# Kernel optimization log

Hardware: AMD Instinct MI355X
Metric: run time of the kernel (lower is better)

The kernel has to match this reference:

```python
import jax, jax.numpy as jnp
import numpy as np

N_NODES = 100000
D = 128
N_EDGES = 800000


def setup_inputs() -> dict:
    key = jax.random.key(0)
    k_feat, k_src, k_dst, k_ws, k_wn = jax.random.split(key, 5)
    scale = 1.0 / np.sqrt(D)
    return {
        "features": jax.random.normal(k_feat, (N_NODES, D), jnp.float32),
        "src": jax.random.randint(k_src, (N_EDGES,), 0, N_NODES, jnp.int32),
        "dst": jax.random.randint(k_dst, (N_EDGES,), 0, N_NODES, jnp.int32),
        "gamma": jnp.ones((D,), jnp.float32),
        "beta": jnp.zeros((D,), jnp.float32),
        "W_self": jax.random.normal(k_ws, (D, D), jnp.float32) * scale,
        "W_neigh": jax.random.normal(k_wn, (D, D), jnp.float32) * scale,
        "b": jnp.zeros((D,), jnp.float32),
    }


def reference(features, src, dst, gamma, beta, W_self, W_neigh, b):
    n = features.shape[0]
    eps = 1e-5
    # BatchNorm1d (training mode: batch stats over the node dim, biased var)
    mean = jnp.mean(features, axis=0)
    var = jnp.mean(jnp.square(features - mean), axis=0)
    h = (features - mean) * jax.lax.rsqrt(var + eps) * gamma + beta  # [N, D]

    # SAGEConv 'mean': gather source feats along edges, mean-reduce per dst node
    msg = h[src]  # [E, D] irregular gather
    agg = jax.ops.segment_sum(msg, dst, num_segments=n)  # [N, D]
    deg = jax.ops.segment_sum(jnp.ones(src.shape, h.dtype), dst, num_segments=n)
    h_neigh = agg / jnp.maximum(deg, 1.0)[:, None]  # zero-degree nodes stay 0

    conv = h @ W_self + h_neigh @ W_neigh + b  # fc_self + fc_neigh + bias
    out = conv + h  # skip connection
    return jax.nn.gelu(out, approximate=False)
```

## Files before the change

kernel.cpp:

```cpp
#include <hip/hip_runtime.h>

#define DD 128
#define NPB_LOG 8
#define NPB 256
#define EPB 2048

typedef __attribute__((ext_vector_type(8))) short short8;
typedef __attribute__((ext_vector_type(4))) float f32x4;
typedef __attribute__((ext_vector_type(2))) float f32x2;

__device__ inline unsigned short f2bf(float f) {
    unsigned u = __float_as_uint(f);
    unsigned r = u + 0x7fffu + ((u >> 16) & 1u);
    return (unsigned short)(r >> 16);
}
__device__ inline float bf2f(unsigned short s) {
    return __uint_as_float(((unsigned)s) << 16);
}

__global__ __launch_bounds__(256) void phase1_k(
    const float4* __restrict__ x, float* __restrict__ stats16, int n,
    const int* __restrict__ dst, int nE, int NCHUNK, int NBUCK,
    const float* __restrict__ Wself, const float* __restrict__ Wneigh,
    unsigned short* __restrict__ Bpre, int* __restrict__ cm) {
    int b = blockIdx.x, tid = threadIdx.x;
    __shared__ float ls[8][256];
    if (b < 16) {
        int q = b * 256 + tid;
        int l = q & 63;
        int kb = ((q >> 9) << 5) + ((l >> 4) << 3);
        int nn = (((q >> 6) & 7) << 4) + (l & 15);
        bool self = (kb < 128);
        const float* Wp = self ? (Wself + (size_t)kb * 128 + nn)
                               : (Wneigh + (size_t)(kb - 128) * 128 + nn);
        unsigned tmp[4];
#pragma unroll
        for (int j = 0; j < 4; ++j) {
            float v0 = Wp[(2 * j) * 128];
            float v1 = Wp[(2 * j + 1) * 128];
            if (self) {
                if (kb + 2 * j == nn) v0 += 1.0f;
                if (kb + 2 * j + 1 == nn) v1 += 1.0f;
            }
            tmp[j] = (unsigned)f2bf(v0) | ((unsigned)f2bf(v1) << 16);
        }
        uint4 w; w.x = tmp[0]; w.y = tmp[1]; w.z = tmp[2]; w.w = tmp[3];
        *(uint4*)(Bpre + (size_t)q * 8) = w;
    } else if (b < 16 + 1024) {
        int bb = b - 16;
        int c4 = tid & 31, sub = tid >> 5;
        float sx = 0.f, sy = 0.f, sz = 0.f, sw = 0.f;
        float qx = 0.f, qy = 0.f, qz = 0.f, qw = 0.f;
        for (int r = bb * 8 + sub; r < n; r += 1024 * 8) {
            float4 v = x[(size_t)r * 32 + c4];
            sx += v.x; sy += v.y; sz += v.z; sw += v.w;
            qx += v.x * v.x; qy += v.y * v.y; qz += v.z * v.z; qw += v.w * v.w;
        }
        ls[sub][c4 * 4 + 0] = sx; ls[sub][c4 * 4 + 1] = sy;
        ls[sub][c4 * 4 + 2] = sz; ls[sub][c4 * 4 + 3] = sw;
        ls[sub][128 + c4 * 4 + 0] = qx; ls[sub][128 + c4 * 4 + 1] = qy;
        ls[sub][128 + c4 * 4 + 2] = qz; ls[sub][128 + c4 * 4 + 3] = qw;
        __syncthreads();
        float t = 0.f;
#pragma unroll
        for (int k = 0; k < 8; ++k) t += ls[k][tid];
        atomicAdd(&stats16[(bb & 15) * 256 + tid], t);
    } else {
        int chunk = b - 1040;
        int* cnt = (int*)ls;
        for (int i = tid; i < NBUCK; i += 256) cnt[i] = 0;
        __syncthreads();
        int e0 = chunk * EPB;
#pragma unroll
        for (int j = 0; j < 8; ++j) {
            int e = e0 + j * 256 + tid;
            if (e < nE) atomicAdd(&cnt[dst[e] >> NPB_LOG], 1);
        }
        __syncthreads();
        for (int bk = tid; bk < NBUCK; bk += 256)
            cm[(size_t)bk * NCHUNK + chunk] = cnt[bk];
    }
}

__global__ __launch_bounds__(256) void scanA_k(
    const int* __restrict__ v_in, int* __restrict__ bsum, int n) {
    int b = blockIdx.x, t = threadIdx.x;
    int i0 = b * 1024 + t * 4;
    int4 v = {0, 0, 0, 0};
    if (i0 + 3 < n) v = *(const int4*)(v_in + i0);
    else {
        if (i0 < n) v.x = v_in[i0];
        if (i0 + 1 < n) v.y = v_in[i0 + 1];
        if (i0 + 2 < n) v.z = v_in[i0 + 2];
    }
    __shared__ int ls[256];
    ls[t] = v.x + v.y + v.z + v.w;
    __syncthreads();
#pragma unroll
    for (int off = 128; off > 0; off >>= 1) {
        if (t < off) ls[t] += ls[t + off];
        __syncthreads();
    }
    if (t == 0) bsum[b] = ls[0];
}

__global__ __launch_bounds__(256) void scanB_k(
    const int* __restrict__ bsum, int* __restrict__ bpref,
    int* __restrict__ total_out, int nb, int n) {
    __shared__ int ls[256];
    int t = threadIdx.x;
    ls[t] = (t < nb) ? bsum[t] : 0;
    __syncthreads();
#pragma unroll
    for (int off = 1; off < 256; off <<= 1) {
        int x = (t >= off) ? ls[t - off] : 0;
        __syncthreads();
        ls[t] += x;
        __syncthreads();
    }
    if (t < nb) bpref[t] = (t == 0) ? 0 : ls[t - 1];
    if (t == nb - 1) total_out[n] = ls[t];
}

__global__ __launch_bounds__(256) void scanC_k(
    const int* __restrict__ v_in, const int* __restrict__ bpref,
    int* __restrict__ o1, int* __restrict__ o2, int n) {
    int b = blockIdx.x, t = threadIdx.x;
    int i0 = b * 1024 + t * 4;
    int4 v = {0, 0, 0, 0};
    if (i0 + 3 < n) v = *(const int4*)(v_in + i0);
    else {
        if (i0 < n) v.x = v_in[i0];
        if (i0 + 1 < n) v.y = v_in[i0 + 1];
        if (i0 + 2 < n) v.z = v_in[i0 + 2];
    }
    int s = v.x + v.y + v.z + v.w;
    __shared__ int ls[256];
    ls[t] = s;
    __syncthreads();
#pragma unroll
    for (int off = 1; off < 256; off <<= 1) {
        int x = (t >= off) ? ls[t - off] : 0;
        __syncthreads();
        ls[t] += x;
        __syncthreads();
    }
    int run = bpref[b] + ((t == 0) ? 0 : ls[t - 1]);
    int4 o;
    o.x = run; o.y = run + v.x; o.z = o.y + v.y; o.w = o.z + v.z;
    if (i0 + 3 < n) {
        *(int4*)(o1 + i0) = o;
        *(int4*)(o2 + i0) = o;
    } else {
        if (i0 < n) { o1[i0] = o.x; o2[i0] = o.x; }
        if (i0 + 1 < n) { o1[i0 + 1] = o.y; o2[i0 + 1] = o.y; }
        if (i0 + 2 < n) { o1[i0 + 2] = o.z; o2[i0 + 2] = o.z; }
    }
}

__global__ __launch_bounds__(256) void phase2_k(
    const float4* __restrict__ x, const float* __restrict__ stats16,
    const float4* __restrict__ gamma, const float4* __restrict__ beta,
    uint2* __restrict__ hbuf, unsigned* __restrict__ h8, int n, float inv_n,
    int nbNorm, const int* __restrict__ src, const int* __restrict__ dst,
    const int* __restrict__ cmscan, unsigned* __restrict__ pairs,
    int nE, int NCHUNK, int NBUCK) {
    int b = blockIdx.x, tid = threadIdx.x;
    __shared__ int shr[512];
    if (b < nbNorm) {
        float* fs = (float*)shr;
        float a = 0.f;
#pragma unroll
        for (int sh = 0; sh < 16; ++sh) a += stats16[sh * 256 + tid];
        fs[tid] = a;
        __syncthreads();
        int c4 = tid & 31, sub = tid >> 5;
        int row = b * 8 + sub;
        float4 sm = ((const float4*)fs)[c4], sq = ((const float4*)fs)[32 + c4];
        float4 g = gamma[c4], bt = beta[c4];
        float mx = sm.x * inv_n, my = sm.y * inv_n, mz = sm.z * inv_n, mw = sm.w * inv_n;
        float vx = sq.x * inv_n - mx * mx, vy = sq.y * inv_n - my * my;
        float vz = sq.z * inv_n - mz * mz, vw = sq.w * inv_n - mw * mw;
        float scx = rsqrtf(vx + 1e-5f) * g.x, scy = rsqrtf(vy + 1e-5f) * g.y;
        float scz = rsqrtf(vz + 1e-5f) * g.z, scw = rsqrtf(vw + 1e-5f) * g.w;
        float shx = bt.x - mx * scx, shy = bt.y - my * scy;
        float shz = bt.z - mz * scz, shw = bt.w - mw * scw;
        if (row < n) {
            float4 v = x[(size_t)row * 32 + c4];
            float hx = v.x * scx + shx, hy = v.y * scy + shy;
            float hz = v.z * scz + shz, hw = v.w * scw + shw;
            uint2 o;
            o.x = (unsigned)f2bf(hx) | ((unsigned)f2bf(hy) << 16);
            o.y = (unsigned)f2bf(hz) | ((unsigned)f2bf(hw) << 16);
            hbuf[(size_t)row * 32 + c4] = o;
            int p8 = __builtin_amdgcn_cvt_pk_fp8_f32(hx, hy, 0, false);
            p8 = __builtin_amdgcn_cvt_pk_fp8_f32(hz, hw, p8, true);
            h8[(size_t)row * 32 + c4] = (unsigned)p8;
        }
    } else {
        int chunk = b - nbNorm;
        for (int i = tid; i < NBUCK; i += 256)
            shr[i] = cmscan[(size_t)i * NCHUNK + chunk];
        __syncthreads();
        int e0 = chunk * EPB;
#pragma unroll
        for (int j = 0; j < 8; ++j) {
            int e = e0 + j * 256 + tid;
            if (e < nE) {
                int d = dst[e];
                int p = atomicAdd(&shr[d >> NPB_LOG], 1);
                pairs[p] = ((unsigned)src[e] << NPB_LOG) | (unsigned)(d & (NPB - 1));
            }
        }
    }
}

__global__ __launch_bounds__(256) void sortC_k(
    const unsigned* __restrict__ pairs, const int* __restrict__ cmscan,
    int* __restrict__ offsets, int* __restrict__ csr,
    int n, int nE, int NCHUNK, int NBUCK) {
    int b = blockIdx.x, tid = threadIdx.x;
    int base0 = cmscan[(size_t)b * NCHUNK];
    int end = (b + 1 < NBUCK) ? cmscan[(size_t)(b + 1) * NCHUNK] : nE;
    __shared__ int cnt[NPB];
    __shared__ int cur[NPB];
    cnt[tid] = 0;
    __syncthreads();
    for (int e = base0 + tid; e < end; e += 256)
        atomicAdd(&cnt[pairs[e] & (NPB - 1)], 1);
    __syncthreads();
    int c0 = cnt[tid];
    __shared__ int ps[256];
    ps[tid] = c0;
    __syncthreads();
#pragma unroll
    for (int off = 1; off < 256; off <<= 1) {
        int v = (tid >= off) ? ps[tid - off] : 0;
        __syncthreads();
        ps[tid] += v;
        __syncthreads();
    }
    int ex = base0 + ps[tid] - c0;
    cur[tid] = ex;
    int node = b * NPB + tid;
    if (node < n) offsets[node] = ex;
    if (b == NBUCK - 1 && tid == 0) offsets[n] = nE;
    __syncthreads();
    for (int e = base0 + tid; e < end; e += 256) {
        unsigned u = pairs[e];
        int p = atomicAdd(&cur[u & (NPB - 1)], 1);
        csr[p] = (int)(u >> NPB_LOG);
    }
}

__global__ __launch_bounds__(256) void pull_k(
    const int* __restrict__ offsets, const int* __restrict__ csr,
    const unsigned short* __restrict__ h8u, unsigned* __restrict__ hnw, int n) {
    int wid = (blockIdx.x * 256 + threadIdx.x) >> 6;
    int lane = threadIdx.x & 63;
    if (wid >= n) return;
    int b0 = offsets[wid], b1 = offsets[wid + 1];
    float a0 = 0.f, a1 = 0.f;
    int j = b0;
    for (; j + 8 <= b1; j += 8) {
        unsigned short u[8];
#pragma unroll
        for (int q = 0; q < 8; ++q) u[q] = h8u[(size_t)csr[j + q] * 64 + lane];
#pragma unroll
        for (int q = 0; q < 8; ++q) {
            f32x2 fv = __builtin_amdgcn_cvt_pk_f32_fp8((unsigned)u[q], false);
            a0 += fv.x; a1 += fv.y;
        }
    }
    for (; j + 2 <= b1; j += 2) {
        unsigned short u0 = h8u[(size_t)csr[j] * 64 + lane];
        unsigned short u1 = h8u[(size_t)csr[j + 1] * 64 + lane];
        f32x2 f0 = __builtin_amdgcn_cvt_pk_f32_fp8((unsigned)u0, false);
        f32x2 f1 = __builtin_amdgcn_cvt_pk_f32_fp8((unsigned)u1, false);
        a0 += f0.x + f1.x; a1 += f0.y + f1.y;
    }
    if (j < b1) {
        unsigned short u0 = h8u[(size_t)csr[j] * 64 + lane];
        f32x2 f0 = __builtin_amdgcn_cvt_pk_f32_fp8((unsigned)u0, false);
        a0 += f0.x; a1 += f0.y;
    }
    float rd = (b1 > b0) ? 1.0f / (float)(b1 - b0) : 0.0f;
    unsigned o = (unsigned)f2bf(a0 * rd) | ((unsigned)f2bf(a1 * rd) << 16);
    hnw[(size_t)wid * 64 + lane] = o;
}

__global__ __launch_bounds__(256, 4) void gemm_k(
    const unsigned short* __restrict__ h, const unsigned short* __restrict__ hn,
    const unsigned short* __restrict__ Bpre, const float* __restrict__ bias,
    float* __restrict__ out, int n) {
    __shared__ unsigned short Bsw[16384];
    int tid = threadIdx.x, wave = tid >> 6, lane = tid & 63;
    int H = blockIdx.x & 1, rb = blockIdx.x >> 1;
#pragma unroll
    for (int i = 0; i < 8; ++i) {
        int g = wave * 8 + i;
        int s = g >> 2, tt = g & 3;
        __builtin_amdgcn_global_load_lds(
            (const __attribute__((address_space(1))) void*)(
                Bpre + ((size_t)((s * 8 + H * 4 + tt) * 64) + lane) * 8),
            (__attribute__((address_space(3))) void*)(Bsw + (size_t)g * 512),
            16, 0, 0);
    }
    __syncthreads();

    int quad = lane >> 4, mrow = lane & 15;
    int r0 = rb * 128 + wave * 32;
    int rA0 = min(r0 + mrow, n - 1);
    int rA1 = min(r0 + 16 + mrow, n - 1);

    f32x4 zero = {0.0f, 0.0f, 0.0f, 0.0f};
    f32x4 acc[2][4];
#pragma unroll
    for (int m = 0; m < 2; ++m)
#pragma unroll
        for (int t = 0; t < 4; ++t) acc[m][t] = zero;

#pragma unroll
    for (int s = 0; s < 8; ++s) {
        int kb = s * 32 + quad * 8;
        short8 a0, a1;
        if (s < 4) {
            a0 = *(const short8*)(h + (size_t)rA0 * 128 + kb);
            a1 = *(const short8*)(h + (size_t)rA1 * 128 + kb);
        } else {
            int kk = kb - 128;
            a0 = *(const short8*)(hn + (size_t)rA0 * 128 + kk);
            a1 = *(const short8*)(hn + (size_t)rA1 * 128 + kk);
        }
#pragma unroll
        for (int tt = 0; tt < 4; ++tt) {
            short8 b = *(const short8*)(Bsw + ((size_t)(s * 4 + tt) * 64 + lane) * 8);
            acc[0][tt] = __builtin_amdgcn_mfma_f32_16x16x32_bf16(a0, b, acc[0][tt], 0, 0, 0);
            acc[1][tt] = __builtin_amdgcn_mfma_f32_16x16x32_bf16(a1, b, acc[1][tt], 0, 0, 0);
        }
    }

    float bi[4];
#pragma unroll
    for (int t = 0; t < 4; ++t) bi[t] = bias[H * 64 + t * 16 + mrow];
#pragma unroll
    for (int m = 0; m < 2; ++m) {
#pragma unroll
        for (int i = 0; i < 4; ++i) {
            int row = r0 + m * 16 + quad * 4 + i;
            if (row < n) {
#pragma unroll
                for (int t = 0; t < 4; ++t) {
                    int col = H * 64 + t * 16 + mrow;
                    float xv = acc[m][t][i] + bi[t];
                    float x2 = xv * xv;
                    float u = 0.7978845608f * xv * (1.0f + 0.044715f * x2);
                    float e = __expf(2.0f * u);
                    float th = 1.0f - 2.0f * __builtin_amdgcn_rcpf(e + 1.0f);
                    out[(size_t)row * 128 + col] = 0.5f * xv * (1.0f + th);
                }
            }
        }
    }
}

extern "C" void kernel_launch(void* const* d_in, const int* in_sizes, int n_in,
                              void* d_out, int out_size, void* d_ws, size_t ws_size,
                              hipStream_t stream) {
    const float* features = (const float*)d_in[0];
    const int* src = (const int*)d_in[1];
    const int* dst = (const int*)d_in[2];
    const float* gamma = (const float*)d_in[3];
    const float* beta = (const float*)d_in[4];
    const float* Wself = (const float*)d_in[5];
    const float* Wneigh = (const float*)d_in[6];
    const float* bias = (const float*)d_in[7];
    int n = in_sizes[0] / DD;
    int nE = in_sizes[1];
    int NCHUNK = (nE + EPB - 1) / EPB;
    int NBUCK = (n + NPB - 1) / NPB;
    int CM = NBUCK * NCHUNK;
    int tilesCM = (CM + 1023) / 1024;
    int nbNorm = (n + 7) / 8;

    auto align1k = [](size_t x) { return (x + 1023) & ~(size_t)1023; };
    char* ws = (char*)d_ws;
    size_t off = 0;
    float* stats16 = (float*)(ws + off);       off += 16384;
    int* cm       = (int*)(ws + off);          off += align1k((size_t)(CM + 1) * 4);
    int* cmscan   = (int*)(ws + off);          off += align1k((size_t)CM * 4);
    int* offsets  = (int*)(ws + off);          off += align1k((size_t)(n + 1) * 4);
    int* csr      = (int*)(ws + off);          off += align1k((size_t)nE * 4);
    unsigned* pairs = (unsigned*)(ws + off);   off += align1k((size_t)nE * 4);
    int* bsum     = (int*)(ws + off);          off += 1024;
    int* bpref    = (int*)(ws + off);          off += 1024;
    unsigned short* Bpre = (unsigned short*)(ws + off); off += 65536;
    unsigned short* hbuf = (unsigned short*)(ws + off); off += (size_t)n * 256;
    unsigned short* hnbuf = (unsigned short*)(ws + off); off += (size_t)n * 256;
    unsigned* h8 = (unsigned*)(ws + off);      off += (size_t)n * 128;

    hipMemsetAsync(stats16, 0, 16384, stream);

    phase1_k<<<16 + 1024 + NCHUNK, 256, 0, stream>>>(
        (const float4*)features, stats16, n, dst, nE, NCHUNK, NBUCK,
        Wself, Wneigh, Bpre, cm);
    scanA_k<<<tilesCM, 256, 0, stream>>>(cm, bsum, CM);
    scanB_k<<<1, 256, 0, stream>>>(bsum, bpref, cm, tilesCM, CM);
    scanC_k<<<tilesCM, 256, 0, stream>>>(cm, bpref, cmscan, cmscan, CM);
    phase2_k<<<nbNorm + NCHUNK, 256, 0, stream>>>(
        (const float4*)features, stats16, (const float4*)gamma,
        (const float4*)beta, (uint2*)hbuf, h8, n, 1.0f / (float)n, nbNorm,
        src, dst, cmscan, pairs, nE, NCHUNK, NBUCK);
    sortC_k<<<NBUCK, 256, 0, stream>>>(pairs, cmscan, offsets, csr, n, nE,
                                       NCHUNK, NBUCK);
    pull_k<<<(n * 64 + 255) / 256, 256, 0, stream>>>(
        offsets, csr, (const unsigned short*)h8, (unsigned*)hnbuf, n);
    gemm_k<<<((n + 127) / 128) * 2, 256, 0, stream>>>(
        hbuf, hnbuf, Bpre, bias, (float*)d_out, n);
}
```

Baseline: 226.3 us.

## Pack eight nodes per wave in neighbor pull with 16-byte fp8 loads

The neighbor-mean gather now gives each node 8 lanes instead of a full 64-lane wave. Each lane loads 16 bytes (16 fp8 values) per neighbor and writes 32 bytes of bf16 output, so a wave serves 8 nodes at once. This is meant to cut the per-wave setup and scalar overhead and to issue wider, fewer memory transactions for the short neighbor lists (about 8 edges per node on average). The cost is more registers per lane and divergence between the 8 node groups in a wave when their degrees differ.

```diff
diff --git a/kernel.cpp b/kernel.cpp
--- a/kernel.cpp
+++ b/kernel.cpp
@@ -253,40 +253,64 @@
     }
 }
 
+#define ACC8(v)                                                       \
+    do {                                                              \
+        acc[0] += __builtin_amdgcn_cvt_pk_f32_fp8((v).x, false);      \
+        acc[1] += __builtin_amdgcn_cvt_pk_f32_fp8((v).x, true);       \
+        acc[2] += __builtin_amdgcn_cvt_pk_f32_fp8((v).y, false);      \
+        acc[3] += __builtin_amdgcn_cvt_pk_f32_fp8((v).y, true);       \
+        acc[4] += __builtin_amdgcn_cvt_pk_f32_fp8((v).z, false);      \
+        acc[5] += __builtin_amdgcn_cvt_pk_f32_fp8((v).z, true);       \
+        acc[6] += __builtin_amdgcn_cvt_pk_f32_fp8((v).w, false);      \
+        acc[7] += __builtin_amdgcn_cvt_pk_f32_fp8((v).w, true);       \
+    } while (0)
+
 __global__ __launch_bounds__(256) void pull_k(
     const int* __restrict__ offsets, const int* __restrict__ csr,
-    const unsigned short* __restrict__ h8u, unsigned* __restrict__ hnw, int n) {
-    int wid = (blockIdx.x * 256 + threadIdx.x) >> 6;
+    const uint4* __restrict__ h8q, uint4* __restrict__ hnw, int n) {
+    int wv = (blockIdx.x * 256 + threadIdx.x) >> 6;
     int lane = threadIdx.x & 63;
-    if (wid >= n) return;
-    int b0 = offsets[wid], b1 = offsets[wid + 1];
-    float a0 = 0.f, a1 = 0.f;
+    int g = lane >> 3, sl = lane & 7;
+    int node = wv * 8 + g;
+    bool valid = node < n;
+    int nc = valid ? node : (n - 1);
+    int b0 = offsets[nc], b1 = offsets[nc + 1];
+    f32x2 acc[8];
+#pragma unroll
+    for (int k = 0; k < 8; ++k) acc[k] = f32x2{0.f, 0.f};
     int j = b0;
-    for (; j + 8 <= b1; j += 8) {
-        unsigned short u[8];
-#pragma unroll
-        for (int q = 0; q < 8; ++q) u[q] = h8u[(size_t)csr[j + q] * 64 + lane];
-#pragma unroll
-        for (int q = 0; q < 8; ++q) {
-            f32x2 fv = __builtin_amdgcn_cvt_pk_f32_fp8((unsigned)u[q], false);
-            a0 += fv.x; a1 += fv.y;
-        }
-    }
-    for (; j + 2 <= b1; j += 2) {
-        unsigned short u0 = h8u[(size_t)csr[j] * 64 + lane];
-        unsigned short u1 = h8u[(size_t)csr[j + 1] * 64 + lane];
-        f32x2 f0 = __builtin_amdgcn_cvt_pk_f32_fp8((unsigned)u0, false);
-        f32x2 f1 = __builtin_amdgcn_cvt_pk_f32_fp8((unsigned)u1, false);
-        a0 += f0.x + f1.x; a1 += f0.y + f1.y;
+    for (; j + 4 <= b1; j += 4) {
+        int i0 = csr[j], i1 = csr[j + 1], i2 = csr[j + 2], i3 = csr[j + 3];
+        uint4 v0 = h8q[(size_t)i0 * 8 + sl];
+        uint4 v1 = h8q[(size_t)i1 * 8 + sl];
+        uint4 v2 = h8q[(size_t)i2 * 8 + sl];
+        uint4 v3 = h8q[(size_t)i3 * 8 + sl];
+        ACC8(v0); ACC8(v1); ACC8(v2); ACC8(v3);
+    }
+    if (j + 2 <= b1) {
+        int i0 = csr[j], i1 = csr[j + 1];
+        uint4 v0 = h8q[(size_t)i0 * 8 + sl];
+        uint4 v1 = h8q[(size_t)i1 * 8 + sl];
+        ACC8(v0); ACC8(v1);
+        j += 2;
     }
     if (j < b1) {
-        unsigned short u0 = h8u[(size_t)csr[j] * 64 + lane];
-        f32x2 f0 = __builtin_amdgcn_cvt_pk_f32_fp8((unsigned)u0, false);
-        a0 += f0.x; a1 += f0.y;
-    }
-    float rd = (b1 > b0) ? 1.0f / (float)(b1 - b0) : 0.0f;
-    unsigned o = (unsigned)f2bf(a0 * rd) | ((unsigned)f2bf(a1 * rd) << 16);
-    hnw[(size_t)wid * 64 + lane] = o;
+        int i0 = csr[j];
+        uint4 v0 = h8q[(size_t)i0 * 8 + sl];
+        ACC8(v0);
+    }
+    if (valid) {
+        float rd = (b1 > b0) ? 1.0f / (float)(b1 - b0) : 0.0f;
+        unsigned ow[8];
+#pragma unroll
+        for (int k = 0; k < 8; ++k)
+            ow[k] = (unsigned)f2bf(acc[k].x * rd) |
+                    ((unsigned)f2bf(acc[k].y * rd) << 16);
+        uint4 o1; o1.x = ow[0]; o1.y = ow[1]; o1.z = ow[2]; o1.w = ow[3];
+        uint4 o2; o2.x = ow[4]; o2.y = ow[5]; o2.z = ow[6]; o2.w = ow[7];
+        hnw[(size_t)node * 16 + sl * 2] = o1;
+        hnw[(size_t)node * 16 + sl * 2 + 1] = o2;
+    }
 }
 
 __global__ __launch_bounds__(256, 4) void gemm_k(
@@ -413,8 +437,12 @@
         src, dst, cmscan, pairs, nE, NCHUNK, NBUCK);
     sortC_k<<<NBUCK, 256, 0, stream>>>(pairs, cmscan, offsets, csr, n, nE,
                                        NCHUNK, NBUCK);
-    pull_k<<<(n * 64 + 255) / 256, 256, 0, stream>>>(
-        offsets, csr, (const unsigned short*)h8, (unsigned*)hnbuf, n);
+    {
+        int waves = (n + 7) / 8;
+        int blocks = (waves * 64 + 255) / 256;
+        pull_k<<<blocks, 256, 0, stream>>>(
+            offsets, csr, (const uint4*)h8, (uint4*)hnbuf, n);
+    }
     gemm_k<<<((n + 127) / 128) * 2, 256, 0, stream>>>(
         hbuf, hnbuf, Bpre, bias, (float*)d_out, n);
 }
```

After: 207.8 us. -8.1%, faster.
